# Performance work log

Hardware: AMD Instinct MI355X
Metric: run time of the kernel (lower is better)

## Reference

```python
import jax, jax.numpy as jnp
import numpy as np

B = 4096   # batch_size from init_kwargs
D = 128    # embedding dim
TEMP = 0.25


def _l2_normalize(x, eps=1e-12):
    # matches F.normalize(dim=1): x / max(||x||, eps)
    n = jnp.linalg.norm(x, axis=1, keepdims=True)
    return x / jnp.maximum(n, eps)


def setup_inputs() -> dict:
    key = jax.random.key(0)
    k1, k2 = jax.random.split(key)
    return {
        "emb_i": jax.random.normal(k1, (B, D), dtype=jnp.float32),
        "emb_j": jax.random.normal(k2, (B, D), dtype=jnp.float32),
    }


def reference(emb_i, emb_j):
    b = emb_i.shape[0]
    z_i = _l2_normalize(emb_i)
    z_j = _l2_normalize(emb_j)
    reps = jnp.concatenate([z_i, z_j], axis=0)            # [2B, D]
    # cosine similarity of normalized vectors == dot product
    sim = reps @ reps.T                                    # [2B, 2B]
    sim_ij = jnp.diagonal(sim, offset=b)                   # [B]
    sim_ji = jnp.diagonal(sim, offset=-b)                  # [B]
    positives = jnp.concatenate([sim_ij, sim_ji], axis=0)  # [2B]
    # negatives_mask as overwritten in __init__: ones only on the two
    # off-diagonal cross-view blocks.
    mask = (
        jnp.zeros((2 * b, 2 * b), dtype=sim.dtype)
        .at[:b, b:].set(1.0)
        .at[b:, :b].set(1.0)
    )
    exp_sim = jnp.exp(sim / TEMP)                          # [2B, 2B]
    denom = jnp.sum(mask * exp_sim, axis=1)                # [2B]
    loss_partial = -jnp.log(jnp.exp(positives / TEMP) / denom)
    loss = jnp.sum(loss_partial) / (2 * b)
    return loss
```

## Files before the change

### kernel.cpp

```cpp
#include <hip/hip_runtime.h>

#define BATCH 4096
#define DIM   128
#define NT    32
#define EXP_SCALE 5.770780163555854f

typedef __bf16 bf16_t;
typedef __bf16 bf16x8 __attribute__((ext_vector_type(8)));
typedef float  f32x4  __attribute__((ext_vector_type(4)));

__global__ __launch_bounds__(256) void normalize_kernel(
    const float* __restrict__ emb_i, const float* __restrict__ emb_j,
    bf16_t* __restrict__ zi, bf16_t* __restrict__ zj, float* __restrict__ pos,
    float* __restrict__ denoms )
{
    if (blockIdx.x < 8) {
        int idx = (blockIdx.x * 256 + threadIdx.x) * 4;
        *(float4*)&denoms[idx] = make_float4(0.f, 0.f, 0.f, 0.f);
    }

    int wave = threadIdx.x >> 6;
    int lane = threadIdx.x & 63;
    int k = blockIdx.x * 4 + wave;

    const float2* ei = (const float2*)(emb_i + (size_t)k * DIM);
    const float2* ej = (const float2*)(emb_j + (size_t)k * DIM);
    float2 a = ei[lane];
    float2 b = ej[lane];

    float sii = a.x * a.x + a.y * a.y;
    float sjj = b.x * b.x + b.y * b.y;
    float sij = a.x * b.x + a.y * b.y;
#pragma unroll
    for (int m = 1; m < 64; m <<= 1) {
        sii += __shfl_xor(sii, m);
        sjj += __shfl_xor(sjj, m);
        sij += __shfl_xor(sij, m);
    }
    float inv_i = 1.0f / fmaxf(sqrtf(sii), 1e-12f);
    float inv_j = 1.0f / fmaxf(sqrtf(sjj), 1e-12f);

    struct bf16_2 { bf16_t x, y; };
    bf16_2 pi, pj;
    pi.x = (bf16_t)(a.x * inv_i);  pi.y = (bf16_t)(a.y * inv_i);
    pj.x = (bf16_t)(b.x * inv_j);  pj.y = (bf16_t)(b.y * inv_j);
    ((bf16_2*)(zi + (size_t)k * DIM))[lane] = pi;
    ((bf16_2*)(zj + (size_t)k * DIM))[lane] = pj;

    if (lane == 0) pos[k] = sij * inv_i * inv_j;
}

__global__ __launch_bounds__(256) void gemm_exp_kernel(
    const bf16_t* __restrict__ zi, const bf16_t* __restrict__ zj,
    float* __restrict__ rowDenom, float* __restrict__ colDenom)
{
    __shared__ __align__(16) bf16_t zi_s[128][136];
    __shared__ __align__(16) bf16_t zj_s[128][136];
    __shared__ float colRed[4][128];

    const int tid = threadIdx.x;

    const int orig = blockIdx.x;
    const int swz  = ((orig & 7) << 7) | (orig >> 3);
    const int ti = swz & 31;
    const int tj = swz >> 5;

#pragma unroll
    for (int it = 0; it < 8; ++it) {
        int c = it * 256 + tid;
        int row = c >> 4;
        int col = (c & 15) << 3;
        *(uint4*)&zi_s[row][col] =
            *(const uint4*)(zi + ((size_t)(ti * 128 + row)) * DIM + col);
        *(uint4*)&zj_s[row][col] =
            *(const uint4*)(zj + ((size_t)(tj * 128 + row)) * DIM + col);
    }
    __syncthreads();

    const int wave = tid >> 6;
    const int lane = tid & 63;
    const int l15  = lane & 15;
    const int quad = lane >> 4;

    const f32x4 vzero = {0.f, 0.f, 0.f, 0.f};
    f32x4 acc[2][8];
#pragma unroll
    for (int rt = 0; rt < 2; ++rt)
#pragma unroll
        for (int ct = 0; ct < 8; ++ct) acc[rt][ct] = vzero;

#pragma unroll
    for (int ks = 0; ks < 4; ++ks) {
        int k0 = ks * 32 + quad * 8;
        bf16x8 afrag[2], bfrag[8];
#pragma unroll
        for (int rt = 0; rt < 2; ++rt)
            afrag[rt] = *(const bf16x8*)&zi_s[(wave * 2 + rt) * 16 + l15][k0];
#pragma unroll
        for (int ct = 0; ct < 8; ++ct)
            bfrag[ct] = *(const bf16x8*)&zj_s[ct * 16 + l15][k0];
#pragma unroll
        for (int rt = 0; rt < 2; ++rt)
#pragma unroll
            for (int ct = 0; ct < 8; ++ct)
                acc[rt][ct] = __builtin_amdgcn_mfma_f32_16x16x32_bf16(
                    afrag[rt], bfrag[ct], acc[rt][ct], 0, 0, 0);
    }

    float rowPart[2][4] = {{0.f, 0.f, 0.f, 0.f}, {0.f, 0.f, 0.f, 0.f}};
    float colPart[8]    = {0.f, 0.f, 0.f, 0.f, 0.f, 0.f, 0.f, 0.f};
#pragma unroll
    for (int rt = 0; rt < 2; ++rt)
#pragma unroll
        for (int ct = 0; ct < 8; ++ct)
#pragma unroll
            for (int r = 0; r < 4; ++r) {
                float e = exp2f(acc[rt][ct][r] * EXP_SCALE);
                rowPart[rt][r] += e;
                colPart[ct]    += e;
            }

#pragma unroll
    for (int rt = 0; rt < 2; ++rt)
#pragma unroll
        for (int r = 0; r < 4; ++r) {
            float v = rowPart[rt][r];
            v += __shfl_xor(v, 1);
            v += __shfl_xor(v, 2);
            v += __shfl_xor(v, 4);
            v += __shfl_xor(v, 8);
            if (l15 == 0) {
                int grow = ti * 128 + (wave * 2 + rt) * 16 + quad * 4 + r;
                atomicAdd(&rowDenom[grow], v);
            }
        }

#pragma unroll
    for (int ct = 0; ct < 8; ++ct) {
        float v = colPart[ct];
        v += __shfl_xor(v, 16);
        v += __shfl_xor(v, 32);
        if (quad == 0) colRed[wave][ct * 16 + l15] = v;
    }
    __syncthreads();
    if (tid < 128) {
        float s = colRed[0][tid] + colRed[1][tid] + colRed[2][tid] + colRed[3][tid];
        atomicAdd(&colDenom[tj * 128 + tid], s);
    }
}

__global__ __launch_bounds__(256) void finalize_kernel(
    const float* __restrict__ denoms, const float* __restrict__ pos,
    float* __restrict__ out)
{
    const float* rowDenom = denoms;
    const float* colDenom = denoms + BATCH;
    int tid = threadIdx.x;
    float acc = 0.f;
#pragma unroll
    for (int it = 0; it < 16; ++it) {
        int k = it * 256 + tid;
        acc += logf(rowDenom[k]) + logf(colDenom[k]) - 8.0f * pos[k];
    }
#pragma unroll
    for (int m = 1; m < 64; m <<= 1) acc += __shfl_xor(acc, m);
    __shared__ float red[4];
    if ((tid & 63) == 0) red[tid >> 6] = acc;
    __syncthreads();
    if (tid == 0)
        out[0] = (red[0] + red[1] + red[2] + red[3]) * (1.0f / (2.0f * BATCH));
}

extern "C" void kernel_launch(void* const* d_in, const int* in_sizes, int n_in,
                              void* d_out, int out_size, void* d_ws, size_t ws_size,
                              hipStream_t stream) {
    const float* emb_i = (const float*)d_in[0];
    const float* emb_j = (const float*)d_in[1];
    float* out = (float*)d_out;

    char* ws = (char*)d_ws;
    bf16_t* zi     = (bf16_t*)(ws);
    bf16_t* zj     = (bf16_t*)(ws + (1u << 20));
    float*  denoms = (float*)(ws + (2u << 20));
    float*  pos    = denoms + 2 * BATCH;

    normalize_kernel<<<BATCH / 4, 256, 0, stream>>>(emb_i, emb_j, zi, zj, pos, denoms);
    gemm_exp_kernel<<<1024, 256, 0, stream>>>(zi, zj, denoms, denoms + BATCH);
    finalize_kernel<<<1, 256, 0, stream>>>(denoms, pos, out);
}
```

Measured before the change: 75.58 us.

## Replace atomic denominator accumulation with per-tile partial buffers and parallel finalize

The GEMM kernel now writes per-tile row and column partial sums into dedicated buffers instead of issuing global float atomicAdds. The finalize kernel is spread over 16 blocks, each summing 32 partials per element before the log, and the blocks combine their results with one atomic into the output, which the normalize kernel zeroes. The block-index swizzle is dropped in favour of a plain 2D grid. This removes atomic contention and the single-block finalize, at the cost of extra partial-buffer traffic and possibly worse L2 locality without the swizzle.

```diff
diff --git a/kernel.cpp b/kernel.cpp
--- a/kernel.cpp
+++ b/kernel.cpp
@@ -12,12 +12,9 @@
 __global__ __launch_bounds__(256) void normalize_kernel(
     const float* __restrict__ emb_i, const float* __restrict__ emb_j,
     bf16_t* __restrict__ zi, bf16_t* __restrict__ zj, float* __restrict__ pos,
-    float* __restrict__ denoms )
+    float* __restrict__ out)
 {
-    if (blockIdx.x < 8) {
-        int idx = (blockIdx.x * 256 + threadIdx.x) * 4;
-        *(float4*)&denoms[idx] = make_float4(0.f, 0.f, 0.f, 0.f);
-    }
+    if (blockIdx.x == 0 && threadIdx.x == 0) out[0] = 0.0f;
 
     int wave = threadIdx.x >> 6;
     int lane = threadIdx.x & 63;
@@ -52,18 +49,16 @@
 
 __global__ __launch_bounds__(256) void gemm_exp_kernel(
     const bf16_t* __restrict__ zi, const bf16_t* __restrict__ zj,
-    float* __restrict__ rowDenom, float* __restrict__ colDenom)
+    float* __restrict__ rowP,
+    float* __restrict__ colP)
 {
     __shared__ __align__(16) bf16_t zi_s[128][136];
     __shared__ __align__(16) bf16_t zj_s[128][136];
     __shared__ float colRed[4][128];
+    __shared__ float rowRed[128];
 
     const int tid = threadIdx.x;
-
-    const int orig = blockIdx.x;
-    const int swz  = ((orig & 7) << 7) | (orig >> 3);
-    const int ti = swz & 31;
-    const int tj = swz >> 5;
+    const int ti = blockIdx.x, tj = blockIdx.y;
 
 #pragma unroll
     for (int it = 0; it < 8; ++it) {
@@ -129,10 +124,8 @@
             v += __shfl_xor(v, 2);
             v += __shfl_xor(v, 4);
             v += __shfl_xor(v, 8);
-            if (l15 == 0) {
-                int grow = ti * 128 + (wave * 2 + rt) * 16 + quad * 4 + r;
-                atomicAdd(&rowDenom[grow], v);
-            }
+            if (l15 == 0)
+                rowRed[(wave * 2 + rt) * 16 + quad * 4 + r] = v;
         }
 
 #pragma unroll
@@ -144,31 +137,32 @@
     }
     __syncthreads();
     if (tid < 128) {
+        rowP[(size_t)tj * BATCH + ti * 128 + tid] = rowRed[tid];
         float s = colRed[0][tid] + colRed[1][tid] + colRed[2][tid] + colRed[3][tid];
-        atomicAdd(&colDenom[tj * 128 + tid], s);
+        colP[(size_t)ti * BATCH + tj * 128 + tid] = s;
     }
 }
 
 __global__ __launch_bounds__(256) void finalize_kernel(
-    const float* __restrict__ denoms, const float* __restrict__ pos,
-    float* __restrict__ out)
+    const float* __restrict__ rowP, const float* __restrict__ colP,
+    const float* __restrict__ pos, float* __restrict__ out)
 {
-    const float* rowDenom = denoms;
-    const float* colDenom = denoms + BATCH;
-    int tid = threadIdx.x;
-    float acc = 0.f;
+    const int k = blockIdx.x * 256 + threadIdx.x;
+    float rd = 0.f, cd = 0.f;
 #pragma unroll
-    for (int it = 0; it < 16; ++it) {
-        int k = it * 256 + tid;
-        acc += logf(rowDenom[k]) + logf(colDenom[k]) - 8.0f * pos[k];
+    for (int t = 0; t < NT; ++t) {
+        rd += rowP[(size_t)t * BATCH + k];
+        cd += colP[(size_t)t * BATCH + k];
     }
+    float v = logf(rd) + logf(cd) - 8.0f * pos[k];
 #pragma unroll
-    for (int m = 1; m < 64; m <<= 1) acc += __shfl_xor(acc, m);
+    for (int m = 1; m < 64; m <<= 1) v += __shfl_xor(v, m);
     __shared__ float red[4];
-    if ((tid & 63) == 0) red[tid >> 6] = acc;
+    if ((threadIdx.x & 63) == 0) red[threadIdx.x >> 6] = v;
     __syncthreads();
-    if (tid == 0)
-        out[0] = (red[0] + red[1] + red[2] + red[3]) * (1.0f / (2.0f * BATCH));
+    if (threadIdx.x == 0)
+        atomicAdd(out, (red[0] + red[1] + red[2] + red[3]) *
+                           (1.0f / (2.0f * BATCH)));
 }
 
 extern "C" void kernel_launch(void* const* d_in, const int* in_sizes, int n_in,
@@ -179,12 +173,13 @@
     float* out = (float*)d_out;
 
     char* ws = (char*)d_ws;
-    bf16_t* zi     = (bf16_t*)(ws);
-    bf16_t* zj     = (bf16_t*)(ws + (1u << 20));
-    float*  denoms = (float*)(ws + (2u << 20));
-    float*  pos    = denoms + 2 * BATCH;
+    bf16_t* zi   = (bf16_t*)(ws);
+    bf16_t* zj   = (bf16_t*)(ws + (1u << 20));
+    float*  rowP = (float*)(ws + (2u << 20));
+    float*  colP = (float*)(ws + (2u << 20) + (512u << 10));
+    float*  pos  = (float*)(ws + (3u << 20));
 
-    normalize_kernel<<<BATCH / 4, 256, 0, stream>>>(emb_i, emb_j, zi, zj, pos, denoms);
-    gemm_exp_kernel<<<1024, 256, 0, stream>>>(zi, zj, denoms, denoms + BATCH);
-    finalize_kernel<<<1, 256, 0, stream>>>(denoms, pos, out);
+    normalize_kernel<<<BATCH / 4, 256, 0, stream>>>(emb_i, emb_j, zi, zj, pos, out);
+    gemm_exp_kernel<<<dim3(NT, NT), 256, 0, stream>>>(zi, zj, rowP, colP);
+    finalize_kernel<<<BATCH / 256, 256, 0, stream>>>(rowP, colP, pos, out);
 }
```

New measurement: 92.23 us. +22.0%, slower.
